# Performance work log

Measured on AMD Instinct MI355X. Metric: run time of the kernel, lower is better.

Reference implementation:

```python
import jax, jax.numpy as jnp
import numpy as np

THRESHOLD = 0.5
NEG_POS_RATIO = 3
ALPHA = 1.0
BETA = 1.0
IGNORE_INDEX = 255

B, P, C, O = 16, 16384, 21, 16
H = W = 256


def cxcy_to_xy(c):
    return jnp.concatenate([c[..., :2] - c[..., 2:] / 2, c[..., :2] + c[..., 2:] / 2], axis=-1)


def xy_to_cxcy(xy):
    return jnp.concatenate([(xy[..., :2] + xy[..., 2:]) / 2, xy[..., 2:] - xy[..., :2]], axis=-1)


def cxcy_to_gcxgcy(cxcy, priors_cxcy):
    return jnp.concatenate([
        (cxcy[..., :2] - priors_cxcy[..., :2]) / (priors_cxcy[..., 2:] / 10.0),
        jnp.log(cxcy[..., 2:] / priors_cxcy[..., 2:]) * 5.0,
    ], axis=-1)


def jaccard(set1, set2):
    # set1 [O,4] xy, set2 [P,4] xy -> IoU [O,P]
    lo = jnp.maximum(set1[:, None, :2], set2[None, :, :2])
    hi = jnp.minimum(set1[:, None, 2:], set2[None, :, 2:])
    wh = jnp.clip(hi - lo, 0.0)
    inter = wh[..., 0] * wh[..., 1]
    a1 = (set1[:, 2] - set1[:, 0]) * (set1[:, 3] - set1[:, 1])
    a2 = (set2[:, 2] - set2[:, 0]) * (set2[:, 3] - set2[:, 1])
    return inter / (a1[:, None] + a2[None, :] - inter)


def setup_inputs() -> dict:
    key = jax.random.key(0)
    ks = jax.random.split(key, 8)
    predicted_locs = jax.random.normal(ks[0], (B, P, 4), dtype=jnp.float32)
    predicted_scores = jax.random.normal(ks[1], (B, P, C), dtype=jnp.float32)
    predicted_masks = jax.random.normal(ks[2], (B, C, H, W), dtype=jnp.float32)
    x1y1 = jax.random.uniform(ks[3], (B, O, 2), dtype=jnp.float32) * 0.8
    wh = jax.random.uniform(ks[4], (B, O, 2), dtype=jnp.float32) * 0.19 + 0.01
    boxes = jnp.concatenate([x1y1, x1y1 + wh], axis=-1)  # valid xy boxes
    pc = jax.random.uniform(ks[5], (P, 2), dtype=jnp.float32) * 0.9 + 0.05
    pwh = jax.random.uniform(ks[6], (P, 2), dtype=jnp.float32) * 0.28 + 0.02
    priors_cxcy = jnp.concatenate([pc, pwh], axis=-1)
    labels = jax.random.randint(ks[7], (B, O), 1, C)  # object labels, never background
    masks = jax.random.randint(jax.random.fold_in(key, 99), (B, 1, H, W), 0, C)
    return {
        'predicted_locs': predicted_locs,
        'predicted_scores': predicted_scores,
        'predicted_masks': predicted_masks,
        'boxes': boxes,
        'priors_cxcy': priors_cxcy,
        'labels': labels,
        'masks': masks,
    }


def _assign(bx, lb, priors_cxcy, priors_xy):
    # bx [O,4] xy, lb [O] int -> true_locs [P,4], true_classes [P]
    ov = jaccard(bx, priors_xy)  # [O,P]
    overlap_for_each_prior = ov.max(axis=0)       # [P]
    object_for_each_prior = ov.argmax(axis=0)     # [P]
    prior_for_each_object = ov.argmax(axis=1)     # [O]
    # guarantee every object is matched to its best prior
    object_for_each_prior = object_for_each_prior.at[prior_for_each_object].set(jnp.arange(O))
    overlap_for_each_prior = overlap_for_each_prior.at[prior_for_each_object].set(1.0)
    label_for_each_prior = lb[object_for_each_prior]
    label_for_each_prior = jnp.where(overlap_for_each_prior < THRESHOLD, 0, label_for_each_prior)
    true_locs = cxcy_to_gcxgcy(xy_to_cxcy(bx[object_for_each_prior]), priors_cxcy)
    return true_locs, label_for_each_prior


def reference(predicted_locs, predicted_scores, predicted_masks, boxes, priors_cxcy, labels, masks):
    priors_xy = cxcy_to_xy(priors_cxcy)
    true_locs, true_classes = jax.vmap(_assign, in_axes=(0, 0, None, None))(
        boxes, labels, priors_cxcy, priors_xy)  # [B,P,4], [B,P]

    pos = true_classes != 0                      # [B,P]
    pos_f = pos.astype(predicted_locs.dtype)
    n_pos = pos.sum(axis=1)                      # [B]

    # localization: L1Loss (mean over positive prior elements)
    diff = jnp.abs(predicted_locs - true_locs)
    loc_loss = (diff * pos_f[..., None]).sum() / jnp.maximum(pos_f.sum() * 4.0, 1.0)

    # confidence: CE per prior + hard negative mining
    logp = jax.nn.log_softmax(predicted_scores, axis=-1)            # [B,P,C]
    ce = -jnp.take_along_axis(logp, true_classes[..., None], axis=-1)[..., 0]  # [B,P]
    ce_pos_sum = (ce * pos_f).sum()
    ce_neg = jnp.where(pos, 0.0, ce)
    ce_neg_sorted = -jnp.sort(-ce_neg, axis=1)                      # descending
    ranks = jnp.arange(P)[None, :]
    hard = (ranks < (NEG_POS_RATIO * n_pos)[:, None]).astype(ce.dtype)
    ce_hardneg_sum = (ce_neg_sorted * hard).sum()
    conf_loss = (ce_hardneg_sum + ce_pos_sum) / n_pos.sum().astype(ce.dtype)

    # mask loss: cross_entropy2d, sum reduction then / (H*W) / B
    tgt = masks[:, 0]                                                # [B,H,W]
    valid = (tgt != IGNORE_INDEX)
    t = jnp.where(valid, tgt, 0)
    logp_m = jax.nn.log_softmax(predicted_masks, axis=1)             # [B,C,H,W]
    ce_m = -jnp.take_along_axis(logp_m, t[:, None], axis=1)[:, 0]    # [B,H,W]
    mask_loss = (ce_m * valid.astype(ce_m.dtype)).sum() / (H * W) / B

    return conf_loss + ALPHA * loc_loss + BETA * mask_loss
```

## Files before the change

kernel.cpp:

```cpp
#include <hip/hip_runtime.h>
#include <cstdint>
#include <cstddef>

#define Bn 16
#define Pn 16384
#define Cn 21
#define On 16
#define HWn 65536
#define THRESH 0.5f


__device__ __forceinline__ float waveReduceSum(float v) {
  for (int off = 32; off > 0; off >>= 1) v += __shfl_down(v, off, 64);
  return v;
}
__device__ __forceinline__ int waveReduceSumI(int v) {
  for (int off = 32; off > 0; off >>= 1) v += __shfl_down(v, off, 64);
  return v;
}

__global__ __launch_bounds__(256) void k_p1mask(
    const float* __restrict__ boxes, const float* __restrict__ priors,
    const float* __restrict__ pm, const int* __restrict__ msk,
    unsigned long long* __restrict__ partials, float* __restrict__ mpart,
    int* __restrict__ done_cnt) {
  const int lane = threadIdx.x & 63, wave = threadIdx.x >> 6;
  __shared__ float4 sbox[On];
  __shared__ float sarea[On];
  __shared__ unsigned long long skey[On];
  __shared__ float sr1[4];

  if (blockIdx.x == 0 && threadIdx.x == 0) *done_cnt = 0;

  if (blockIdx.x >= 1024) {
    const int idx4 = (blockIdx.x - 1024) * 256 + threadIdx.x;
    const int b = idx4 >> 14;
    const int pix = (idx4 & 16383) << 2;
    int4 t4 = ((const int4*)msk)[idx4];
    const float* base = pm + (size_t)b * ((size_t)Cn * HWn) + pix;
#define M_LD(i) (*(const float4*)(base + (size_t)(i) * HWn))
    float4 q0 = M_LD(0), q1 = M_LD(1), q2 = M_LD(2), q3 = M_LD(3);
    float4 q4 = M_LD(4), q5 = M_LD(5), q6 = M_LD(6), q7 = M_LD(7);
    const bool w0 = (t4.x != 255), w1 = (t4.y != 255), w2 = (t4.z != 255),
               w3 = (t4.w != 255);
    const int c0 = w0 ? t4.x : 0, c1 = w1 ? t4.y : 0, c2 = w2 ? t4.z : 0,
              c3 = w3 ? t4.w : 0;
    float s0 = 0.f, s1 = 0.f, s2 = 0.f, s3 = 0.f;
    float x0 = 0.f, x1 = 0.f, x2 = 0.f, x3 = 0.f;
#define M_ACC(v, c)                                                         \
  {                                                                         \
    s0 += __expf(v.x); s1 += __expf(v.y);                                   \
    s2 += __expf(v.z); s3 += __expf(v.w);                                   \
    if (c0 == c) x0 = v.x; if (c1 == c) x1 = v.y;                           \
    if (c2 == c) x2 = v.z; if (c3 == c) x3 = v.w;                           \
  }
#define M_STEP(r, c, pf) { float4 t = r; r = M_LD(pf); M_ACC(t, c) }
    M_STEP(q0, 0, 8)  M_STEP(q1, 1, 9)  M_STEP(q2, 2, 10) M_STEP(q3, 3, 11)
    M_STEP(q4, 4, 12) M_STEP(q5, 5, 13) M_STEP(q6, 6, 14) M_STEP(q7, 7, 15)
    M_STEP(q0, 8, 16) M_STEP(q1, 9, 17) M_STEP(q2, 10, 18) M_STEP(q3, 11, 19)
    M_STEP(q4, 12, 20)
    M_ACC(q5, 13) M_ACC(q6, 14) M_ACC(q7, 15) M_ACC(q0, 16)
    M_ACC(q1, 17) M_ACC(q2, 18) M_ACC(q3, 19) M_ACC(q4, 20)
#undef M_STEP
#undef M_ACC
#undef M_LD
    float contrib = (w0 ? (__logf(s0) - x0) : 0.f) +
                    (w1 ? (__logf(s1) - x1) : 0.f) +
                    (w2 ? (__logf(s2) - x2) : 0.f) +
                    (w3 ? (__logf(s3) - x3) : 0.f);
    float r = waveReduceSum(contrib);
    if (lane == 0) sr1[wave] = r;
    __syncthreads();
    if (threadIdx.x == 0)
      mpart[blockIdx.x - 1024] = sr1[0] + sr1[1] + sr1[2] + sr1[3];
    return;
  }

  const int b = blockIdx.x >> 6;
  const int p0 = (blockIdx.x & 63) << 8;
  const int p = p0 + threadIdx.x;
  if (threadIdx.x < On) {
    float4 bx = ((const float4*)boxes)[b * On + threadIdx.x];
    sbox[threadIdx.x] = bx;
    sarea[threadIdx.x] = (bx.z - bx.x) * (bx.w - bx.y);
    skey[threadIdx.x] = 0ULL;
  }
  __syncthreads();
  float4 pr = ((const float4*)priors)[p];
  const float px1 = pr.x - 0.5f * pr.z, py1 = pr.y - 0.5f * pr.w;
  const float px2 = pr.x + 0.5f * pr.z, py2 = pr.y + 0.5f * pr.w;
  const float parea = pr.z * pr.w;
#pragma unroll
  for (int o = 0; o < On; ++o) {
    float4 bx = sbox[o];
    float ix = fmaxf(fminf(px2, bx.z) - fmaxf(px1, bx.x), 0.f);
    float iy = fmaxf(fminf(py2, bx.w) - fmaxf(py1, bx.y), 0.f);
    float inter = ix * iy;
    float iou = inter / (sarea[o] + parea - inter);
    float m = iou;
#pragma unroll
    for (int off = 32; off > 0; off >>= 1) m = fmaxf(m, __shfl_xor(m, off, 64));
    unsigned long long tie = __ballot(iou == m);
    if (lane == 0) {
      int lmin = __ffsll(tie) - 1;
      unsigned minp = (unsigned)(p0 + (wave << 6) + lmin);
      unsigned long long key = ((unsigned long long)__float_as_uint(m) << 32) |
                               (unsigned long long)(0xFFFFFFFFu - minp);
      atomicMax(&skey[o], key);
    }
  }
  __syncthreads();
  if (threadIdx.x < On)
    partials[(size_t)blockIdx.x * On + threadIdx.x] = skey[threadIdx.x];
}

__global__ __launch_bounds__(256, 2) void k_assign(
    const float* __restrict__ plocs, const float* __restrict__ pscores,
    const float* __restrict__ boxes, const float* __restrict__ priors,
    const int* __restrict__ labels, const unsigned long long* __restrict__ partials,
    float* __restrict__ ce_neg, float* __restrict__ apart_loc,
    float* __restrict__ apart_ce, int* __restrict__ apart_npos) {
  __shared__ float ssc[256 * Cn];
  __shared__ float4 sbox[On];
  __shared__ float sarea[On];
  __shared__ int slab[On];
  __shared__ int spfo[On];
  __shared__ unsigned long long skey[On];
  __shared__ float sr1[4], sr2[4];
  __shared__ int sri[4];
  const int lane = threadIdx.x & 63, wave = threadIdx.x >> 6;
  const int b = blockIdx.x >> 6;
  const int p0 = (blockIdx.x & 63) << 8;
  const int p = p0 + threadIdx.x;
  {
    const float4* src = (const float4*)(pscores + ((size_t)b * Pn + p0) * Cn);
    float4* dst = (float4*)ssc;
#pragma unroll
    for (int i = threadIdx.x; i < (256 * Cn) / 4; i += 256) dst[i] = src[i];
  }
  if (threadIdx.x < On) {
    float4 bx = ((const float4*)boxes)[b * On + threadIdx.x];
    sbox[threadIdx.x] = bx;
    sarea[threadIdx.x] = (bx.z - bx.x) * (bx.w - bx.y);
    slab[threadIdx.x] = labels[b * On + threadIdx.x];
    skey[threadIdx.x] = 0ULL;
  }
  __syncthreads();
  {
    const int o = threadIdx.x & 15, j = threadIdx.x >> 4;
    const unsigned long long* pp = partials + ((size_t)b * 64) * On;
    unsigned long long k = 0ULL;
#pragma unroll
    for (int t = 0; t < 4; ++t) {
      unsigned long long v = pp[(size_t)(j * 4 + t) * On + o];
      k = v > k ? v : k;
    }
    atomicMax(&skey[o], k);
  }
  __syncthreads();
  if (threadIdx.x < On)
    spfo[threadIdx.x] = (int)(0xFFFFFFFFu - (unsigned)(skey[threadIdx.x] & 0xFFFFFFFFULL));
  __syncthreads();

  float4 pr = ((const float4*)priors)[p];
  const float px1 = pr.x - 0.5f * pr.z, py1 = pr.y - 0.5f * pr.w;
  const float px2 = pr.x + 0.5f * pr.z, py2 = pr.y + 0.5f * pr.w;
  const float parea = pr.z * pr.w;
  float best = -1.f;
  int bobj = 0;
#pragma unroll
  for (int o = 0; o < On; ++o) {
    float4 bx = sbox[o];
    float ix = fmaxf(fminf(px2, bx.z) - fmaxf(px1, bx.x), 0.f);
    float iy = fmaxf(fminf(py2, bx.w) - fmaxf(py1, bx.y), 0.f);
    float inter = ix * iy;
    float iou = inter / (sarea[o] + parea - inter);
    if (iou > best) { best = iou; bobj = o; }
  }
#pragma unroll
  for (int o = 0; o < On; ++o) {
    if (spfo[o] == p) { bobj = o; best = 1.0f; }
  }
  const int lbl = (best < THRESH) ? 0 : slab[bobj];
  const bool pos = (lbl != 0);
  float locp = 0.f;
  if (pos) {
    float4 bx = sbox[bobj];
    float cx = 0.5f * (bx.x + bx.z), cy = 0.5f * (bx.y + bx.w);
    float w = bx.z - bx.x, h = bx.w - bx.y;
    float g0 = (cx - pr.x) / (pr.z * 0.1f);
    float g1 = (cy - pr.y) / (pr.w * 0.1f);
    float g2 = logf(w / pr.z) * 5.f;
    float g3 = logf(h / pr.w) * 5.f;
    float4 pl = ((const float4*)plocs)[b * Pn + p];
    locp = fabsf(pl.x - g0) + fabsf(pl.y - g1) + fabsf(pl.z - g2) + fabsf(pl.w - g3);
  }
  const float* my = ssc + threadIdx.x * Cn;
  float s = 0.f, xt = 0.f;
#pragma unroll
  for (int c = 0; c < Cn; ++c) {
    float v = my[c];
    s += __expf(v);
    if (c == lbl) xt = v;
  }
  float ce = __logf(s) - xt;
  ce_neg[b * Pn + p] = pos ? 0.f : ce;
  float cep = pos ? ce : 0.f;

  float r1 = waveReduceSum(locp);
  float r2 = waveReduceSum(cep);
  int ri = waveReduceSumI(pos ? 1 : 0);
  if (lane == 0) { sr1[wave] = r1; sr2[wave] = r2; sri[wave] = ri; }
  __syncthreads();
  if (threadIdx.x == 0) {
    apart_loc[blockIdx.x] = sr1[0] + sr1[1] + sr1[2] + sr1[3];
    apart_ce[blockIdx.x] = sr2[0] + sr2[1] + sr2[2] + sr2[3];
    apart_npos[blockIdx.x] = sri[0] + sri[1] + sri[2] + sri[3];
  }
}

__global__ __launch_bounds__(1024) void k_hardneg_final(
    const float* __restrict__ ce_neg, const int* __restrict__ apart_npos,
    const float* __restrict__ apart_loc, const float* __restrict__ apart_ce,
    const float* __restrict__ mpart, float* __restrict__ bres,
    int* __restrict__ done_cnt, float* __restrict__ out) {
  const int b = blockIdx.x;
  const int tid = threadIdx.x;
  const int lane = tid & 63, wave = tid >> 6;
  __shared__ int scnt[16];
  __shared__ float ssum[16];
  __shared__ int sK;
  unsigned rv[16];
#pragma unroll
  for (int i = 0; i < 16; ++i)
    rv[i] = __float_as_uint(ce_neg[b * Pn + i * 1024 + tid]);
  if (wave == 0) {
    int v = (lane < 64) ? apart_npos[b * 64 + lane] : 0;
    v = waveReduceSumI(v);
    if (lane == 0) sK = v;
  }
  __syncthreads();
  int K = 3 * sK;
  if (K > Pn) K = Pn;
  unsigned lo = 0u, hi = 0x7F800000u;
  while (lo < hi) {
    unsigned mid = lo + ((hi - lo) >> 1);
    int c = 0;
#pragma unroll
    for (int i = 0; i < 16; ++i) c += (rv[i] > mid) ? 1 : 0;
    c = waveReduceSumI(c);
    if (lane == 0) scnt[wave] = c;
    __syncthreads();
    int total = 0;
#pragma unroll
    for (int w = 0; w < 16; ++w) total += scnt[w];
    if (total < K) hi = mid; else lo = mid + 1;
    __syncthreads();
  }
  const float fv = __uint_as_float(lo);
  float s = 0.f;
  int c = 0;
#pragma unroll
  for (int i = 0; i < 16; ++i) {
    if (rv[i] > lo) { s += __uint_as_float(rv[i]); c++; }
  }
  s = waveReduceSum(s);
  c = waveReduceSumI(c);
  if (lane == 0) { ssum[wave] = s; scnt[wave] = c; }
  __syncthreads();
  if (tid == 0) {
    float tots = 0.f;
    int totc = 0;
#pragma unroll
    for (int w = 0; w < 16; ++w) { tots += ssum[w]; totc += scnt[w]; }
    bres[b] = tots + (float)(K - totc) * fv;
  }
  __syncthreads();

  if (tid == 0) {
    __threadfence();
    scnt[0] = atomicAdd(done_cnt, 1);
  }
  __syncthreads();
  if (scnt[0] != Bn - 1) return;
  __threadfence();
  float l_loc = apart_loc[tid];
  float l_ce = apart_ce[tid];
  float l_msk = mpart[tid];
  int l_np = apart_npos[tid];
  float l_hn = (tid < Bn) ? atomicAdd(&bres[tid], 0.f) : 0.f;
  l_loc = waveReduceSum(l_loc);
  l_ce = waveReduceSum(l_ce);
  l_msk = waveReduceSum(l_msk);
  l_hn = waveReduceSum(l_hn);
  int l_npw = waveReduceSumI(l_np);
  if (lane == 0) {
    ssum[wave] = l_loc;
    scnt[wave] = l_npw;
  }
  __syncthreads();
  __shared__ float sce[16], smk[16], shn[16];
  if (lane == 0) { sce[wave] = l_ce; smk[wave] = l_msk; shn[wave] = l_hn; }
  __syncthreads();
  if (tid == 0) {
    float a0 = 0.f, a1 = 0.f, a2 = 0.f, a3 = 0.f;
    int np_i = 0;
#pragma unroll
    for (int w = 0; w < 16; ++w) {
      a0 += ssum[w]; a1 += sce[w]; a3 += smk[w]; a2 += shn[w];
      np_i += scnt[w];
    }
    float np = (float)np_i;
    float conf = (a2 + a1) / np;
    float loc = a0 / fmaxf(np * 4.f, 1.f);
    float maskl = a3 / (float)HWn / (float)Bn;
    out[0] = conf + loc + maskl;
  }
}

extern "C" void kernel_launch(void* const* d_in, const int* in_sizes, int n_in,
                              void* d_out, int out_size, void* d_ws, size_t ws_size,
                              hipStream_t stream) {
  const float* plocs   = (const float*)d_in[0];
  const float* pscores = (const float*)d_in[1];
  const float* pmasks  = (const float*)d_in[2];
  const float* boxes   = (const float*)d_in[3];
  const float* priors  = (const float*)d_in[4];
  const int*   labels  = (const int*)d_in[5];
  const int*   masks   = (const int*)d_in[6];

  char* ws = (char*)d_ws;
  float* mpart = (float*)ws;
  unsigned long long* partials = (unsigned long long*)(ws + 4096);
  float* ce_neg = (float*)(ws + 135168);
  float* apart_loc = (float*)(ws + 1183744);
  float* apart_ce = (float*)(ws + 1187840);
  int* apart_npos = (int*)(ws + 1191936);
  float* bres = (float*)(ws + 1196032);
  int* done_cnt = (int*)(ws + 1196160);

  k_p1mask<<<2048, 256, 0, stream>>>(boxes, priors, pmasks, masks, partials,
                                     mpart, done_cnt);
  k_assign<<<1024, 256, 0, stream>>>(plocs, pscores, boxes, priors, labels,
                                     partials, ce_neg, apart_loc, apart_ce,
                                     apart_npos);
  k_hardneg_final<<<Bn, 1024, 0, stream>>>(ce_neg, apart_npos, apart_loc,
                                           apart_ce, mpart, bres, done_cnt,
                                           (float*)d_out);
}
```

Baseline: 201.0 us.

## Move mask cross-entropy pass into hard-negative kernel to overlap with serial search

Moves the per-pixel mask cross-entropy reduction from the first (IoU matching) kernel into the final hard-negative mining kernel, launched as 256 extra 1024-thread blocks alongside the 16 per-batch search blocks. The goal is to fill the GPU while the few latency-bound binary-search blocks run, instead of leaving it mostly idle. The last-block completion counter now expects all 272 blocks, and mask partials are read through atomics. It risks losing any overlap the mask work previously had with the matching phase, and it uses larger blocks for the streaming work.

```diff
diff --git a/kernel.cpp b/kernel.cpp
--- a/kernel.cpp
+++ b/kernel.cpp
@@ -19,62 +19,14 @@
   return v;
 }
 
-__global__ __launch_bounds__(256) void k_p1mask(
+__global__ __launch_bounds__(256) void k_phase1(
     const float* __restrict__ boxes, const float* __restrict__ priors,
-    const float* __restrict__ pm, const int* __restrict__ msk,
-    unsigned long long* __restrict__ partials, float* __restrict__ mpart,
-    int* __restrict__ done_cnt) {
+    unsigned long long* __restrict__ partials, int* __restrict__ done_cnt) {
   const int lane = threadIdx.x & 63, wave = threadIdx.x >> 6;
   __shared__ float4 sbox[On];
   __shared__ float sarea[On];
   __shared__ unsigned long long skey[On];
-  __shared__ float sr1[4];
-
   if (blockIdx.x == 0 && threadIdx.x == 0) *done_cnt = 0;
-
-  if (blockIdx.x >= 1024) {
-    const int idx4 = (blockIdx.x - 1024) * 256 + threadIdx.x;
-    const int b = idx4 >> 14;
-    const int pix = (idx4 & 16383) << 2;
-    int4 t4 = ((const int4*)msk)[idx4];
-    const float* base = pm + (size_t)b * ((size_t)Cn * HWn) + pix;
-#define M_LD(i) (*(const float4*)(base + (size_t)(i) * HWn))
-    float4 q0 = M_LD(0), q1 = M_LD(1), q2 = M_LD(2), q3 = M_LD(3);
-    float4 q4 = M_LD(4), q5 = M_LD(5), q6 = M_LD(6), q7 = M_LD(7);
-    const bool w0 = (t4.x != 255), w1 = (t4.y != 255), w2 = (t4.z != 255),
-               w3 = (t4.w != 255);
-    const int c0 = w0 ? t4.x : 0, c1 = w1 ? t4.y : 0, c2 = w2 ? t4.z : 0,
-              c3 = w3 ? t4.w : 0;
-    float s0 = 0.f, s1 = 0.f, s2 = 0.f, s3 = 0.f;
-    float x0 = 0.f, x1 = 0.f, x2 = 0.f, x3 = 0.f;
-#define M_ACC(v, c)                                                         \
-  {                                                                         \
-    s0 += __expf(v.x); s1 += __expf(v.y);                                   \
-    s2 += __expf(v.z); s3 += __expf(v.w);                                   \
-    if (c0 == c) x0 = v.x; if (c1 == c) x1 = v.y;                           \
-    if (c2 == c) x2 = v.z; if (c3 == c) x3 = v.w;                           \
-  }
-#define M_STEP(r, c, pf) { float4 t = r; r = M_LD(pf); M_ACC(t, c) }
-    M_STEP(q0, 0, 8)  M_STEP(q1, 1, 9)  M_STEP(q2, 2, 10) M_STEP(q3, 3, 11)
-    M_STEP(q4, 4, 12) M_STEP(q5, 5, 13) M_STEP(q6, 6, 14) M_STEP(q7, 7, 15)
-    M_STEP(q0, 8, 16) M_STEP(q1, 9, 17) M_STEP(q2, 10, 18) M_STEP(q3, 11, 19)
-    M_STEP(q4, 12, 20)
-    M_ACC(q5, 13) M_ACC(q6, 14) M_ACC(q7, 15) M_ACC(q0, 16)
-    M_ACC(q1, 17) M_ACC(q2, 18) M_ACC(q3, 19) M_ACC(q4, 20)
-#undef M_STEP
-#undef M_ACC
-#undef M_LD
-    float contrib = (w0 ? (__logf(s0) - x0) : 0.f) +
-                    (w1 ? (__logf(s1) - x1) : 0.f) +
-                    (w2 ? (__logf(s2) - x2) : 0.f) +
-                    (w3 ? (__logf(s3) - x3) : 0.f);
-    float r = waveReduceSum(contrib);
-    if (lane == 0) sr1[wave] = r;
-    __syncthreads();
-    if (threadIdx.x == 0)
-      mpart[blockIdx.x - 1024] = sr1[0] + sr1[1] + sr1[2] + sr1[3];
-    return;
-  }
 
   const int b = blockIdx.x >> 6;
   const int p0 = (blockIdx.x & 63) << 8;
@@ -219,75 +171,127 @@
   }
 }
 
-__global__ __launch_bounds__(1024) void k_hardneg_final(
+__global__ __launch_bounds__(1024) void k_hnmask_final(
     const float* __restrict__ ce_neg, const int* __restrict__ apart_npos,
     const float* __restrict__ apart_loc, const float* __restrict__ apart_ce,
-    const float* __restrict__ mpart, float* __restrict__ bres,
+    const float* __restrict__ pm, const int* __restrict__ msk,
+    float* __restrict__ bres, float* __restrict__ mpart,
     int* __restrict__ done_cnt, float* __restrict__ out) {
-  const int b = blockIdx.x;
   const int tid = threadIdx.x;
   const int lane = tid & 63, wave = tid >> 6;
   __shared__ int scnt[16];
   __shared__ float ssum[16];
+  __shared__ float sce[16], smk[16], shn[16];
   __shared__ int sK;
-  unsigned rv[16];
-#pragma unroll
-  for (int i = 0; i < 16; ++i)
-    rv[i] = __float_as_uint(ce_neg[b * Pn + i * 1024 + tid]);
-  if (wave == 0) {
-    int v = (lane < 64) ? apart_npos[b * 64 + lane] : 0;
-    v = waveReduceSumI(v);
-    if (lane == 0) sK = v;
-  }
-  __syncthreads();
-  int K = 3 * sK;
-  if (K > Pn) K = Pn;
-  unsigned lo = 0u, hi = 0x7F800000u;
-  while (lo < hi) {
-    unsigned mid = lo + ((hi - lo) >> 1);
+  __shared__ int stick;
+
+  if (blockIdx.x < Bn) {
+    const int b = blockIdx.x;
+    unsigned rv[16];
+#pragma unroll
+    for (int i = 0; i < 16; ++i)
+      rv[i] = __float_as_uint(ce_neg[b * Pn + i * 1024 + tid]);
+    if (wave == 0) {
+      int v = apart_npos[b * 64 + lane];
+      v = waveReduceSumI(v);
+      if (lane == 0) sK = v;
+    }
+    __syncthreads();
+    int K = 3 * sK;
+    if (K > Pn) K = Pn;
+    unsigned lo = 0u, hi = 0x7F800000u;
+    while (lo < hi) {
+      unsigned mid = lo + ((hi - lo) >> 1);
+      int c = 0;
+#pragma unroll
+      for (int i = 0; i < 16; ++i) c += (rv[i] > mid) ? 1 : 0;
+      c = waveReduceSumI(c);
+      if (lane == 0) scnt[wave] = c;
+      __syncthreads();
+      int total = 0;
+#pragma unroll
+      for (int w = 0; w < 16; ++w) total += scnt[w];
+      if (total < K) hi = mid; else lo = mid + 1;
+      __syncthreads();
+    }
+    const float fv = __uint_as_float(lo);
+    float s = 0.f;
     int c = 0;
 #pragma unroll
-    for (int i = 0; i < 16; ++i) c += (rv[i] > mid) ? 1 : 0;
+    for (int i = 0; i < 16; ++i) {
+      if (rv[i] > lo) { s += __uint_as_float(rv[i]); c++; }
+    }
+    s = waveReduceSum(s);
     c = waveReduceSumI(c);
-    if (lane == 0) scnt[wave] = c;
+    if (lane == 0) { ssum[wave] = s; scnt[wave] = c; }
     __syncthreads();
-    int total = 0;
-#pragma unroll
-    for (int w = 0; w < 16; ++w) total += scnt[w];
-    if (total < K) hi = mid; else lo = mid + 1;
+    if (tid == 0) {
+      float tots = 0.f;
+      int totc = 0;
+#pragma unroll
+      for (int w = 0; w < 16; ++w) { tots += ssum[w]; totc += scnt[w]; }
+      bres[b] = tots + (float)(K - totc) * fv;
+    }
+  } else {
+    const int t = blockIdx.x - Bn;
+    const int idx4 = t * 1024 + tid;
+    const int b = idx4 >> 14;
+    const int pix = (idx4 & 16383) << 2;
+    int4 t4 = ((const int4*)msk)[idx4];
+    const float* base = pm + (size_t)b * ((size_t)Cn * HWn) + pix;
+#define M_LD(i) (*(const float4*)(base + (size_t)(i) * HWn))
+    float4 q0 = M_LD(0), q1 = M_LD(1), q2 = M_LD(2), q3 = M_LD(3);
+    float4 q4 = M_LD(4), q5 = M_LD(5), q6 = M_LD(6), q7 = M_LD(7);
+    const bool w0 = (t4.x != 255), w1 = (t4.y != 255), w2 = (t4.z != 255),
+               w3 = (t4.w != 255);
+    const int c0 = w0 ? t4.x : 0, c1 = w1 ? t4.y : 0, c2 = w2 ? t4.z : 0,
+              c3 = w3 ? t4.w : 0;
+    float s0 = 0.f, s1 = 0.f, s2 = 0.f, s3 = 0.f;
+    float x0 = 0.f, x1 = 0.f, x2 = 0.f, x3 = 0.f;
+#define M_ACC(v, c)                                                         \
+  {                                                                         \
+    s0 += __expf(v.x); s1 += __expf(v.y);                                   \
+    s2 += __expf(v.z); s3 += __expf(v.w);                                   \
+    if (c0 == c) x0 = v.x; if (c1 == c) x1 = v.y;                           \
+    if (c2 == c) x2 = v.z; if (c3 == c) x3 = v.w;                           \
+  }
+#define M_STEP(r, c, pf) { float4 tt = r; r = M_LD(pf); M_ACC(tt, c) }
+    M_STEP(q0, 0, 8)  M_STEP(q1, 1, 9)  M_STEP(q2, 2, 10) M_STEP(q3, 3, 11)
+    M_STEP(q4, 4, 12) M_STEP(q5, 5, 13) M_STEP(q6, 6, 14) M_STEP(q7, 7, 15)
+    M_STEP(q0, 8, 16) M_STEP(q1, 9, 17) M_STEP(q2, 10, 18) M_STEP(q3, 11, 19)
+    M_STEP(q4, 12, 20)
+    M_ACC(q5, 13) M_ACC(q6, 14) M_ACC(q7, 15) M_ACC(q0, 16)
+    M_ACC(q1, 17) M_ACC(q2, 18) M_ACC(q3, 19) M_ACC(q4, 20)
+#undef M_STEP
+#undef M_ACC
+#undef M_LD
+    float contrib = (w0 ? (__logf(s0) - x0) : 0.f) +
+                    (w1 ? (__logf(s1) - x1) : 0.f) +
+                    (w2 ? (__logf(s2) - x2) : 0.f) +
+                    (w3 ? (__logf(s3) - x3) : 0.f);
+    float r = waveReduceSum(contrib);
+    if (lane == 0) ssum[wave] = r;
     __syncthreads();
-  }
-  const float fv = __uint_as_float(lo);
-  float s = 0.f;
-  int c = 0;
-#pragma unroll
-  for (int i = 0; i < 16; ++i) {
-    if (rv[i] > lo) { s += __uint_as_float(rv[i]); c++; }
-  }
-  s = waveReduceSum(s);
-  c = waveReduceSumI(c);
-  if (lane == 0) { ssum[wave] = s; scnt[wave] = c; }
-  __syncthreads();
-  if (tid == 0) {
-    float tots = 0.f;
-    int totc = 0;
-#pragma unroll
-    for (int w = 0; w < 16; ++w) { tots += ssum[w]; totc += scnt[w]; }
-    bres[b] = tots + (float)(K - totc) * fv;
-  }
-  __syncthreads();
-
+    if (tid == 0) {
+      float acc = 0.f;
+#pragma unroll
+      for (int w = 0; w < 16; ++w) acc += ssum[w];
+      mpart[t] = acc;
+    }
+  }
+
+  __syncthreads();
   if (tid == 0) {
     __threadfence();
-    scnt[0] = atomicAdd(done_cnt, 1);
-  }
-  __syncthreads();
-  if (scnt[0] != Bn - 1) return;
+    stick = atomicAdd(done_cnt, 1);
+  }
+  __syncthreads();
+  if (stick != Bn + 256 - 1) return;
   __threadfence();
   float l_loc = apart_loc[tid];
   float l_ce = apart_ce[tid];
-  float l_msk = mpart[tid];
   int l_np = apart_npos[tid];
+  float l_msk = (tid < 256) ? atomicAdd(&mpart[tid], 0.f) : 0.f;
   float l_hn = (tid < Bn) ? atomicAdd(&bres[tid], 0.f) : 0.f;
   l_loc = waveReduceSum(l_loc);
   l_ce = waveReduceSum(l_ce);
@@ -296,11 +300,11 @@
   int l_npw = waveReduceSumI(l_np);
   if (lane == 0) {
     ssum[wave] = l_loc;
+    sce[wave] = l_ce;
+    smk[wave] = l_msk;
+    shn[wave] = l_hn;
     scnt[wave] = l_npw;
   }
-  __syncthreads();
-  __shared__ float sce[16], smk[16], shn[16];
-  if (lane == 0) { sce[wave] = l_ce; smk[wave] = l_msk; shn[wave] = l_hn; }
   __syncthreads();
   if (tid == 0) {
     float a0 = 0.f, a1 = 0.f, a2 = 0.f, a3 = 0.f;
@@ -339,12 +343,11 @@
   float* bres = (float*)(ws + 1196032);
   int* done_cnt = (int*)(ws + 1196160);
 
-  k_p1mask<<<2048, 256, 0, stream>>>(boxes, priors, pmasks, masks, partials,
-                                     mpart, done_cnt);
+  k_phase1<<<1024, 256, 0, stream>>>(boxes, priors, partials, done_cnt);
   k_assign<<<1024, 256, 0, stream>>>(plocs, pscores, boxes, priors, labels,
                                      partials, ce_neg, apart_loc, apart_ce,
                                      apart_npos);
-  k_hardneg_final<<<Bn, 1024, 0, stream>>>(ce_neg, apart_npos, apart_loc,
-                                           apart_ce, mpart, bres, done_cnt,
-                                           (float*)d_out);
-}
+  k_hnmask_final<<<Bn + 256, 1024, 0, stream>>>(ce_neg, apart_npos, apart_loc,
+                                                apart_ce, pmasks, masks, bres,
+                                                mpart, done_cnt, (float*)d_out);
+}
```

Result: faster. 195.7 us (-2.6%).
